# Performance work log

Hardware: AMD Instinct MI355X
Metric: run time of the kernel (lower is better)

Reference implementation:

```python
import jax, jax.numpy as jnp
import numpy as np

VOCAB = 32000
D_MODEL = 512
SEQ_TABLE = 2048
EPS = 1e-5


def layer_norm(x, gamma, beta):
    mu = jnp.mean(x, axis=-1, keepdims=True)
    var = jnp.mean(jnp.square(x - mu), axis=-1, keepdims=True)
    return (x - mu) * jax.lax.rsqrt(var + EPS) * gamma + beta


def setup_inputs() -> dict:
    key = jax.random.key(0)
    ks = jax.random.split(key, 12)
    s = 0.02
    d, h, V = D_MODEL, 4 * D_MODEL, VOCAB
    return {
        "x": jax.random.randint(ks[0], (4, 2048), 0, V, dtype=jnp.int64),
        "word_emb": jax.random.normal(ks[1], (V, d), jnp.float32) * s,
        "pos_emb": jax.random.normal(ks[2], (SEQ_TABLE, d), jnp.float32) * s,
        "Wq": jax.random.normal(ks[3], (d, d), jnp.float32) * s,
        "Wk": jax.random.normal(ks[4], (d, d), jnp.float32) * s,
        "Wv": jax.random.normal(ks[5], (d, d), jnp.float32) * s,
        "g1": jnp.ones((d,), jnp.float32),
        "b1": jnp.zeros((d,), jnp.float32),
        "w_ffn1": jax.random.normal(ks[6], (h, d), jnp.float32) * s,
        "b_ffn1": jnp.zeros((h,), jnp.float32),
        "w_ffn2": jax.random.normal(ks[7], (d, h), jnp.float32) * s,
        "b_ffn2": jnp.zeros((d,), jnp.float32),
        "g2": jnp.ones((d,), jnp.float32),
        "b2": jnp.zeros((d,), jnp.float32),
        "w_vocab": jax.random.normal(ks[8], (V, d), jnp.float32) * s,
        "b_vocab": jnp.zeros((V,), jnp.float32),
    }


def reference(x, word_emb, pos_emb, Wq, Wk, Wv, g1, b1,
              w_ffn1, b_ffn1, w_ffn2, b_ffn2, g2, b2, w_vocab, b_vocab):
    B, S = x.shape
    d_k = Wq.shape[0]
    # embeddings: word + learned positional
    emb = word_emb[x] + pos_emb[jnp.arange(S)][None, :, :]  # [B,S,d]
    # single-head causal attention (torch Linear: y = x @ W.T)
    Q = emb @ Wq.T
    K = emb @ Wk.T
    V = emb @ Wv.T
    scores = jnp.einsum('bqd,bkd->bqk', Q, K) / jnp.sqrt(jnp.float32(d_k))
    causal = jnp.tril(jnp.ones((S, S), bool))
    scores = jnp.where(causal[None], scores, -jnp.inf)
    attn = jax.nn.softmax(scores, axis=-1)
    context = jnp.einsum('bqk,bkd->bqd', attn, V)
    out1 = layer_norm(emb + context, g1, b1)
    ffn = jax.nn.relu(out1 @ w_ffn1.T + b_ffn1) @ w_ffn2.T + b_ffn2
    final = layer_norm(out1 + ffn, g2, b2)
    return final @ w_vocab.T + b_vocab  # [B,S,V]
```

## Files before the change

### kernel.cpp

```cpp
#include <hip/hip_runtime.h>
#include <hip/hip_bf16.h>

typedef __bf16 bf16;
typedef __attribute__((ext_vector_type(4))) __bf16 bf16x4;
typedef __attribute__((ext_vector_type(8))) __bf16 bf16x8;
typedef __attribute__((ext_vector_type(4))) float f32x4;

__device__ inline void gload_lds16(const bf16* g, bf16* l) {
    __builtin_amdgcn_global_load_lds(
        (const __attribute__((address_space(1))) void*)g,
        (__attribute__((address_space(3))) void*)l, 16, 0, 0);
}

struct CvtArgs {
    const float* src[6];
    bf16* dst[6];
    long n4[6];
    float scale[6];
};
__global__ void cvt_all(CvtArgs a) {
    int j = blockIdx.y;
    const float* __restrict__ src = a.src[j];
    bf16* __restrict__ dst = a.dst[j];
    long n4 = a.n4[j];
    float sc = a.scale[j];
    long i = (long)blockIdx.x * blockDim.x + threadIdx.x;
    long stride = (long)gridDim.x * blockDim.x;
    for (; i < n4; i += stride) {
        float4 v = ((const float4*)src)[i];
        bf16x4 o = { (bf16)(v.x * sc), (bf16)(v.y * sc), (bf16)(v.z * sc), (bf16)(v.w * sc) };
        ((bf16x4*)dst)[i] = o;
    }
}

__global__ void embed_kernel(const int* __restrict__ x, const float* __restrict__ we,
                             const float* __restrict__ pe, float* __restrict__ emb_f,
                             bf16* __restrict__ emb_b) {
    int row = blockIdx.x;
    int c   = threadIdx.x;
    int tok = x[row];
    int s   = row & 2047;
    float4 w = ((const float4*)we)[(long)tok * 128 + c];
    float4 p = ((const float4*)pe)[(long)s * 128 + c];
    float4 e = { w.x + p.x, w.y + p.y, w.z + p.z, w.w + p.w };
    ((float4*)emb_f)[(long)row * 128 + c] = e;
    bf16x4 eb = { (bf16)e.x, (bf16)e.y, (bf16)e.z, (bf16)e.w };
    ((bf16x4*)emb_b)[(long)row * 128 + c] = eb;
}

template<bool WF32>
__global__ void ln_kernel(const float* __restrict__ a, const float* __restrict__ bres,
                          const float* __restrict__ g, const float* __restrict__ bb,
                          float* __restrict__ of, bf16* __restrict__ ob) {
    int row = blockIdx.x;
    int t   = threadIdx.x;
    float4 xa = ((const float4*)a)[(long)row * 128 + t];
    float4 xb = ((const float4*)bres)[(long)row * 128 + t];
    float4 xv = { xa.x + xb.x, xa.y + xb.y, xa.z + xb.z, xa.w + xb.w };
    float s  = xv.x + xv.y + xv.z + xv.w;
    float sq = xv.x * xv.x + xv.y * xv.y + xv.z * xv.z + xv.w * xv.w;
    #pragma unroll
    for (int o = 32; o > 0; o >>= 1) {
        s  += __shfl_xor(s, o);
        sq += __shfl_xor(sq, o);
    }
    __shared__ float rs[2], rq[2];
    int wid = t >> 6;
    if ((t & 63) == 0) { rs[wid] = s; rq[wid] = sq; }
    __syncthreads();
    s = rs[0] + rs[1]; sq = rq[0] + rq[1];
    float mu   = s * (1.0f / 512.0f);
    float var  = sq * (1.0f / 512.0f) - mu * mu;
    float rstd = rsqrtf(var + 1e-5f);
    float4 gv = ((const float4*)g)[t];
    float4 bv = ((const float4*)bb)[t];
    float4 y = { (xv.x - mu) * rstd * gv.x + bv.x,
                 (xv.y - mu) * rstd * gv.y + bv.y,
                 (xv.z - mu) * rstd * gv.z + bv.z,
                 (xv.w - mu) * rstd * gv.w + bv.w };
    if (WF32) ((float4*)of)[(long)row * 128 + t] = y;
    bf16x4 yb = { (bf16)y.x, (bf16)y.y, (bf16)y.z, (bf16)y.w };
    ((bf16x4*)ob)[(long)row * 128 + t] = yb;
}

__global__ void softmax_causal(const float* __restrict__ sc, bf16* __restrict__ pr) {
    int row = blockIdx.x;
    int z = row >> 11, q = row & 2047;
    const float* srow = sc + ((long)z * 2048 + q) * 2048;
    bf16*        prow = pr + ((long)z * 2048 + q) * 2048;
    int t = threadIdx.x;
    float v[8];
    int c0 = t * 8;
    if (t <= (q >> 3)) {
        float4 v0 = ((const float4*)srow)[t * 2];
        float4 v1 = ((const float4*)srow)[t * 2 + 1];
        v[0] = v0.x; v[1] = v0.y; v[2] = v0.z; v[3] = v0.w;
        v[4] = v1.x; v[5] = v1.y; v[6] = v1.z; v[7] = v1.w;
    } else {
        #pragma unroll
        for (int j = 0; j < 8; j++) v[j] = -1e30f;
    }
    float mx = -1e30f;
    #pragma unroll
    for (int j = 0; j < 8; j++) {
        if (c0 + j > q) v[j] = -1e30f;
        mx = fmaxf(mx, v[j]);
    }
    int lane = t & 63, wid = t >> 6;
    #pragma unroll
    for (int o = 32; o > 0; o >>= 1) mx = fmaxf(mx, __shfl_xor(mx, o));
    __shared__ float redm[4], reds[4];
    if (lane == 0) redm[wid] = mx;
    __syncthreads();
    mx = fmaxf(fmaxf(redm[0], redm[1]), fmaxf(redm[2], redm[3]));
    float p[8]; float sum = 0.f;
    #pragma unroll
    for (int j = 0; j < 8; j++) {
        p[j] = (c0 + j <= q) ? __expf(v[j] - mx) : 0.f;
        sum += p[j];
    }
    #pragma unroll
    for (int o = 32; o > 0; o >>= 1) sum += __shfl_xor(sum, o);
    if (lane == 0) reds[wid] = sum;
    __syncthreads();
    sum = reds[0] + reds[1] + reds[2] + reds[3];
    float inv = 1.0f / sum;
    int wlim = ((q >> 7) + 1) * 128;
    if (c0 < wlim) {
        bf16x8 o;
        #pragma unroll
        for (int j = 0; j < 8; j++) o[j] = (bf16)(p[j] * inv);
        *(bf16x8*)&prow[c0] = o;
    }
}

enum { EPI_F32 = 0, EPI_BF16 = 1, EPI_VT = 2, EPI_BIAS_RELU_BF16 = 3, EPI_BIAS_F32 = 4,
       EPI_QKV = 5, EPI_BIAS_F32_NT = 6 };
enum { ZB_BATCH = 0 };

template<int EPI, bool CAUSAL_SKIP, bool CAUSAL_K, bool XCD, int ZMODE>
__global__ __launch_bounds__(256)
void gemm_bt(const bf16* __restrict__ A, const bf16* __restrict__ B,
             float* __restrict__ Cf, bf16* __restrict__ Cb,
             const float* __restrict__ bias, float scale,
             int M, int N, int K, int Krow, long sA, long sB, long sC) {
    int br, bc;
    if (XCD) {
        int nwg = gridDim.x * gridDim.y;
        int lin = blockIdx.y * gridDim.x + blockIdx.x;
        lin = (lin & 7) * (nwg >> 3) + (lin >> 3);
        br = lin / gridDim.x; bc = lin - br * gridDim.x;
    } else { br = blockIdx.y; bc = blockIdx.x; }
    int z = blockIdx.z;
    A += (long)z * sA; B += (long)z * sB; Cf += (long)z * sC;
    if (CAUSAL_SKIP && bc > br) return;
    int Kext = CAUSAL_K ? min(K, (br + 1) * 128) : K;
    __shared__ bf16 As[128 * 64];
    __shared__ bf16 Bs[128 * 64];
    int tid = threadIdx.x;
    int lane = tid & 63, wid = tid >> 6;
    int wm = (wid >> 1) * 64, wn = (wid & 1) * 64;
    f32x4 acc[4][4] = {};
    int rowA0 = br * 128, colB0 = bc * 128;
    int rsub = lane >> 3;
    int csub = ((lane & 7) ^ rsub) * 8;
    int rdsw = (lane & 7) * 8;
    for (int kt = 0; kt < Kext; kt += 64) {
        const bf16* Ag = A + (long)rowA0 * Krow + kt;
        const bf16* Bg = B + (long)colB0 * Krow + kt;
        #pragma unroll
        for (int i = 0; i < 4; i++) {
            int seg = wid * 4 + i;
            int r = seg * 8 + rsub;
            gload_lds16(&Ag[(long)r * Krow + csub], &As[seg * 512]);
            gload_lds16(&Bg[(long)r * Krow + csub], &Bs[seg * 512]);
        }
        __syncthreads();
        #pragma unroll
        for (int kk = 0; kk < 2; kk++) {
            bf16x8 af[4], bfr[4];
            int ko = (kk * 32 + (lane >> 4) * 8) ^ rdsw;
            #pragma unroll
            for (int m = 0; m < 4; m++) af[m]  = *(const bf16x8*)&As[(wm + m * 16 + (lane & 15)) * 64 + ko];
            #pragma unroll
            for (int n = 0; n < 4; n++) bfr[n] = *(const bf16x8*)&Bs[(wn + n * 16 + (lane & 15)) * 64 + ko];
            #pragma unroll
            for (int m = 0; m < 4; m++)
                #pragma unroll
                for (int n = 0; n < 4; n++)
                    acc[m][n] = __builtin_amdgcn_mfma_f32_16x16x32_bf16(af[m], bfr[n], acc[m][n], 0, 0, 0);
        }
        __syncthreads();
    }
    #pragma unroll
    for (int m = 0; m < 4; m++) {
        #pragma unroll
        for (int n = 0; n < 4; n++) {
            #pragma unroll
            for (int j = 0; j < 4; j++) {
                int row = rowA0 + wm + m * 16 + (lane >> 4) * 4 + j;
                int col = colB0 + wn + n * 16 + (lane & 15);
                float v = acc[m][n][j];
                if (EPI == EPI_F32) {
                    Cf[(long)row * N + col] = v;
                } else if (EPI == EPI_BF16) {
                    Cb[(long)row * N + col] = (bf16)(v * scale);
                } else if (EPI == EPI_VT) {
                    int b = row >> 11, k = row & 2047;
                    Cb[((long)b * 512 + col) * 2048 + k] = (bf16)v;
                } else if (EPI == EPI_BIAS_RELU_BF16) {
                    float y = fmaxf(v + bias[col], 0.0f);
                    Cb[(long)row * N + col] = (bf16)y;
                } else if (EPI == EPI_BIAS_F32) {
                    Cf[(long)row * N + col] = v + bias[col];
                }
            }
        }
    }
}

template<int EPI, bool XCD, bool CSKIP, int BANDW, int NT>
__global__ __launch_bounds__(512)
void gemm256(const bf16* __restrict__ A, const bf16* __restrict__ B,
             float* __restrict__ Cf, bf16* __restrict__ Cb,
             const float* __restrict__ bias, int N, int K,
             long sA, long sB, long sC) {
    int br, bc;
    if (XCD) {
        int nwg = gridDim.x * gridDim.y;
        int lin = blockIdx.y * gridDim.x + blockIdx.x;
        lin = (lin & 7) * (nwg >> 3) + (lin >> 3);
        if (BANDW > 0) {
            int per = BANDW * gridDim.y;
            int band = lin / per, w2 = lin - band * per;
            br = w2 / BANDW; bc = band * BANDW + (w2 - br * BANDW);
        } else {
            br = lin / gridDim.x; bc = lin - br * gridDim.x;
        }
    } else { br = blockIdx.y; bc = blockIdx.x; }
    if (CSKIP && bc > br) return;
    int z = blockIdx.z;
    A  += (long)z * sA;
    B  += (long)z * sB;
    Cf += (long)z * sC;
    __shared__ bf16 lds[2][2][256 * 64];
    int tid = threadIdx.x;
    int lane = tid & 63, wid = tid >> 6;
    int wm2 = wid >> 2, wn4 = wid & 3;
    long rowA0 = (long)br * 256, colB0 = (long)bc * 256;
    int rsub = lane >> 3;
    int csw  = ((lane & 7) ^ rsub) * 8;
    int l15 = lane & 15;
    int rdxor = (lane & 7) << 3;
    int kbase = (lane >> 4) * 8;
    const bf16* Abase = A + rowA0 * K;
    const bf16* Bbase = B + colB0 * K;
    f32x4 acc[8][4] = {};

    auto stage = [&](int t) {
        int buf = t & 1;
        const bf16* Ag = Abase + t * 64;
        const bf16* Bg = Bbase + t * 64;
        #pragma unroll
        for (int i = 0; i < 4; i++) {
            int seg = wid * 4 + i;
            long r = seg * 8 + rsub;
            gload_lds16(&Ag[r * K + csw], &lds[buf][0][seg * 512]);
        }
        #pragma unroll
        for (int i = 0; i < 4; i++) {
            int seg = wid * 4 + i;
            long r = seg * 8 + rsub;
            gload_lds16(&Bg[r * K + csw], &lds[buf][1][seg * 512]);
        }
    };

    stage(0);
    stage(1);

    for (int t = 0; t < NT; t++) {
        int buf = t & 1;
        if (t == NT - 1) asm volatile("s_waitcnt vmcnt(0)" ::: "memory");
        else             asm volatile("s_waitcnt vmcnt(8)" ::: "memory");
        __builtin_amdgcn_s_barrier();
        const bf16* As = lds[buf][0];
        const bf16* Bs = lds[buf][1];
        bf16x8 bfr[2][4], af[2][4];
        #pragma unroll
        for (int kk = 0; kk < 2; kk++)
            #pragma unroll
            for (int n = 0; n < 4; n++) {
                int r = wn4 * 64 + n * 16 + l15;
                bfr[kk][n] = *(const bf16x8*)&Bs[r * 64 + ((kk * 32 + kbase) ^ rdxor)];
            }
        #pragma unroll
        for (int kk = 0; kk < 2; kk++)
            #pragma unroll
            for (int m = 0; m < 4; m++) {
                int r = wm2 * 128 + m * 16 + l15;
                af[kk][m] = *(const bf16x8*)&As[r * 64 + ((kk * 32 + kbase) ^ rdxor)];
            }
        __builtin_amdgcn_s_setprio(1);
        #pragma unroll
        for (int kk = 0; kk < 2; kk++)
            #pragma unroll
            for (int m = 0; m < 4; m++)
                #pragma unroll
                for (int n = 0; n < 4; n++)
                    acc[m][n] = __builtin_amdgcn_mfma_f32_16x16x32_bf16(af[kk][m], bfr[kk][n], acc[m][n], 0, 0, 0);
        __builtin_amdgcn_s_setprio(0);
        #pragma unroll
        for (int kk = 0; kk < 2; kk++)
            #pragma unroll
            for (int m = 0; m < 4; m++) {
                int r = wm2 * 128 + 64 + m * 16 + l15;
                af[kk][m] = *(const bf16x8*)&As[r * 64 + ((kk * 32 + kbase) ^ rdxor)];
            }
        asm volatile("s_waitcnt lgkmcnt(0)" ::: "memory");
        __builtin_amdgcn_sched_barrier(0);
        __builtin_amdgcn_s_barrier();
        if (t + 2 < NT) stage(t + 2);
        __builtin_amdgcn_s_setprio(1);
        #pragma unroll
        for (int kk = 0; kk < 2; kk++)
            #pragma unroll
            for (int m = 0; m < 4; m++)
                #pragma unroll
                for (int n = 0; n < 4; n++)
                    acc[4 + m][n] = __builtin_amdgcn_mfma_f32_16x16x32_bf16(af[kk][m], bfr[kk][n], acc[4 + m][n], 0, 0, 0);
        __builtin_amdgcn_s_setprio(0);
    }

    if constexpr (EPI == EPI_QKV) {
        int region = (int)(colB0 >> 9);
        if (region < 2) {
            bf16* dst = Cb + (long)region * (8192L * 512);
            int cb = ((int)colB0 & 511) + wn4 * 64;
            #pragma unroll
            for (int m = 0; m < 8; m++)
                #pragma unroll
                for (int n = 0; n < 4; n++)
                    #pragma unroll
                    for (int j = 0; j < 4; j++) {
                        long row = rowA0 + wm2 * 128 + m * 16 + (lane >> 4) * 4 + j;
                        int c = cb + n * 16 + l15;
                        dst[row * 512 + c] = (bf16)acc[m][n][j];
                    }
        } else {
            bf16* vtb = Cb + 2L * 8192 * 512;
            int cb = ((int)colB0 - 1024) + wn4 * 64;
            #pragma unroll
            for (int m = 0; m < 8; m++)
                #pragma unroll
                for (int n = 0; n < 4; n++) {
                    long k0 = rowA0 + wm2 * 128 + m * 16 + (lane >> 4) * 4;
                    long b = k0 >> 11, k = k0 & 2047;
                    int c = cb + n * 16 + l15;
                    bf16x4 pk = { (bf16)acc[m][n][0], (bf16)acc[m][n][1],
                                  (bf16)acc[m][n][2], (bf16)acc[m][n][3] };
                    *(bf16x4*)&vtb[(b * 512 + c) * 2048 + k] = pk;
                }
        }
    } else {
        #pragma unroll
        for (int m = 0; m < 8; m++) {
            #pragma unroll
            for (int n = 0; n < 4; n++) {
                #pragma unroll
                for (int j = 0; j < 4; j++) {
                    long row = rowA0 + wm2 * 128 + m * 16 + (lane >> 4) * 4 + j;
                    long col = colB0 + wn4 * 64 + n * 16 + l15;
                    float v = acc[m][n][j];
                    if (EPI == EPI_BIAS_F32) {
                        Cf[row * N + col] = v + bias[col];
                    } else if (EPI == EPI_BIAS_F32_NT) {
                        __builtin_nontemporal_store(v + bias[col], &Cf[row * N + col]);
                    } else if (EPI == EPI_BIAS_RELU_BF16) {
                        Cb[row * N + col] = (bf16)fmaxf(v + bias[col], 0.0f);
                    } else if (EPI == EPI_F32) {
                        Cf[row * N + col] = v;
                    }
                }
            }
        }
    }
}

extern "C" void kernel_launch(void* const* d_in, const int* in_sizes, int n_in,
                              void* d_out, int out_size, void* d_ws, size_t ws_size,
                              hipStream_t stream) {
    const int*   x       = (const int*)d_in[0];
    const float* word_emb = (const float*)d_in[1];
    const float* pos_emb  = (const float*)d_in[2];
    const float* Wq = (const float*)d_in[3];
    const float* Wk = (const float*)d_in[4];
    const float* Wv = (const float*)d_in[5];
    const float* g1 = (const float*)d_in[6];
    const float* b1 = (const float*)d_in[7];
    const float* w_ffn1 = (const float*)d_in[8];
    const float* b_ffn1 = (const float*)d_in[9];
    const float* w_ffn2 = (const float*)d_in[10];
    const float* b_ffn2 = (const float*)d_in[11];
    const float* g2 = (const float*)d_in[12];
    const float* b2 = (const float*)d_in[13];
    const float* w_vocab = (const float*)d_in[14];
    const float* b_vocab = (const float*)d_in[15];
    float* out = (float*)d_out;

    char* w = (char*)d_ws;
    auto alloc = [&](size_t bytes) { char* p = w; w += (bytes + 255) & ~255ULL; return p; };
    bf16* wqb   = (bf16*)alloc(512 * 512 * 2);
    bf16* wkb   = (bf16*)alloc(512 * 512 * 2);
    bf16* wvb   = (bf16*)alloc(512 * 512 * 2);
    bf16* w1b   = (bf16*)alloc(2048 * 512 * 2);
    bf16* w2b   = (bf16*)alloc(512 * 2048 * 2);
    bf16* wvocb = (bf16*)alloc((size_t)32000 * 512 * 2);
    float* embf = (float*)alloc((size_t)8192 * 512 * 4);
    bf16* embb  = (bf16*)alloc((size_t)8192 * 512 * 2);
    bf16* qb    = (bf16*)alloc((size_t)8192 * 512 * 2);
    bf16* kb    = (bf16*)alloc((size_t)8192 * 512 * 2);
    bf16* vt    = (bf16*)alloc((size_t)8192 * 512 * 2);
    float* scores = (float*)alloc((size_t)4 * 2048 * 2048 * 4);
    bf16* probs = (bf16*)alloc((size_t)4 * 2048 * 2048 * 2);
    float* ctx  = (float*)alloc((size_t)8192 * 512 * 4);
    float* out1f = (float*)alloc((size_t)8192 * 512 * 4);
    float* ffn2f = (float*)alloc((size_t)8192 * 512 * 4);
    bf16* ffn1b = (bf16*)scores;
    bf16* out1b = kb;
    bf16* finalb = embb;

    const float qscale = 0.044194173824159216f;

    CvtArgs ca;
    ca.src[0] = Wq;      ca.dst[0] = wqb;   ca.n4[0] = 512 * 512 / 4;          ca.scale[0] = qscale;
    ca.src[1] = Wk;      ca.dst[1] = wkb;   ca.n4[1] = 512 * 512 / 4;          ca.scale[1] = 1.0f;
    ca.src[2] = Wv;      ca.dst[2] = wvb;   ca.n4[2] = 512 * 512 / 4;          ca.scale[2] = 1.0f;
    ca.src[3] = w_ffn1;  ca.dst[3] = w1b;   ca.n4[3] = 2048 * 512 / 4;         ca.scale[3] = 1.0f;
    ca.src[4] = w_ffn2;  ca.dst[4] = w2b;   ca.n4[4] = 512 * 2048 / 4;         ca.scale[4] = 1.0f;
    ca.src[5] = w_vocab; ca.dst[5] = wvocb; ca.n4[5] = (long)32000 * 512 / 4;  ca.scale[5] = 1.0f;
    cvt_all<<<dim3(256, 6), 256, 0, stream>>>(ca);

    embed_kernel<<<8192, 128, 0, stream>>>(x, word_emb, pos_emb, embf, embb);

    gemm256<EPI_QKV, true, false, 0, 8><<<dim3(6, 32, 1), 512, 0, stream>>>(
        embb, wqb, nullptr, qb, nullptr, 1536, 512, 0, 0, 0);

    gemm256<EPI_F32, true, true, 0, 8><<<dim3(8, 8, 4), 512, 0, stream>>>(
        qb, kb, scores, nullptr, nullptr, 2048, 512,
        (long)2048 * 512, (long)2048 * 512, (long)2048 * 2048);

    softmax_causal<<<8192, 256, 0, stream>>>(scores, probs);

    gemm_bt<EPI_F32, false, true, false, ZB_BATCH><<<dim3(4, 16, 4), 256, 0, stream>>>(
        probs, vt, ctx, nullptr, nullptr, 1.0f, 2048, 512, 2048, 2048,
        (long)2048 * 2048, (long)512 * 2048, (long)2048 * 512);

    ln_kernel<true><<<8192, 128, 0, stream>>>(embf, ctx, g1, b1, out1f, out1b);

    gemm256<EPI_BIAS_RELU_BF16, true, false, 0, 8><<<dim3(8, 32, 1), 512, 0, stream>>>(
        out1b, w1b, nullptr, ffn1b, b_ffn1, 2048, 512, 0, 0, 0);

    gemm_bt<EPI_BIAS_F32, false, false, false, ZB_BATCH><<<dim3(4, 64, 1), 256, 0, stream>>>(
        ffn1b, w2b, ffn2f, nullptr, b_ffn2, 1.0f, 8192, 512, 2048, 2048, 0, 0, 0);

    ln_kernel<false><<<8192, 128, 0, stream>>>(out1f, ffn2f, g2, b2, nullptr, finalb);

    gemm256<EPI_BIAS_F32_NT, true, false, 5, 8><<<dim3(125, 32, 1), 512, 0, stream>>>(
        finalb, wvocb, out, nullptr, b_vocab, 32000, 512, 0, 0, 0);
}
```

Before: 582.0 us.

## Replace vocab projection GEMM with 128x128-tile kernel using banded tile swizzle

Adds a dedicated 128x128-tile bf16 MFMA GEMM for the final vocab projection. It uses double-buffered direct global-to-LDS loads with XOR swizzling and a block remapping that groups tiles into column bands across XCDs. It replaces the 256-wide tile kernel, which launched 4000 workgroups of 512 threads, with 16000 smaller workgroups to improve occupancy, load balance and L2 reuse of the weight matrix. The trade-off is smaller tiles, which means more redundant A/B traffic per output.

Result: faster. 553.8 us (-4.8%).

```diff
diff --git a/kernel.cpp b/kernel.cpp
--- a/kernel.cpp
+++ b/kernel.cpp
@@ -386,6 +386,97 @@
     }
 }
 
+template<int BANDB>
+__global__ __launch_bounds__(256)
+void gemm128v(const bf16* __restrict__ A, const bf16* __restrict__ B,
+              float* __restrict__ C, const float* __restrict__ bias,
+              int N, int K) {
+    const int NBR = 64;
+    const int NT  = 8;
+    int nwg = gridDim.x;
+    int lin = blockIdx.x;
+    lin = (lin & 7) * (nwg >> 3) + (lin >> 3);
+    int per = BANDB * NBR;
+    int band = lin / per, w2 = lin - band * per;
+    int br = w2 / BANDB, bc = band * BANDB + (w2 - br * BANDB);
+
+    __shared__ bf16 lds[2][2][128 * 64];
+    int tid = threadIdx.x;
+    int lane = tid & 63, wid = tid >> 6;
+    int wm = (wid >> 1) * 64, wn = (wid & 1) * 64;
+    int rsub = lane >> 3;
+    int csub = ((lane & 7) ^ rsub) * 8;
+    int rdsw = (lane & 7) * 8;
+    long rowA0 = (long)br * 128, colB0 = (long)bc * 128;
+    const bf16* Abase = A + rowA0 * K;
+    const bf16* Bbase = B + colB0 * K;
+    f32x4 acc[4][4] = {};
+
+    auto stage = [&](int t) {
+        int buf = t & 1;
+        const bf16* Ag = Abase + t * 64;
+        const bf16* Bg = Bbase + t * 64;
+        #pragma unroll
+        for (int i = 0; i < 4; i++) {
+            int seg = wid * 4 + i;
+            long r = seg * 8 + rsub;
+            gload_lds16(&Ag[r * K + csub], &lds[buf][0][seg * 512]);
+        }
+        #pragma unroll
+        for (int i = 0; i < 4; i++) {
+            int seg = wid * 4 + i;
+            long r = seg * 8 + rsub;
+            gload_lds16(&Bg[r * K + csub], &lds[buf][1][seg * 512]);
+        }
+    };
+
+    stage(0);
+    stage(1);
+
+    for (int t = 0; t < NT; t++) {
+        int buf = t & 1;
+        if (t == NT - 1) asm volatile("s_waitcnt vmcnt(0)" ::: "memory");
+        else             asm volatile("s_waitcnt vmcnt(8)" ::: "memory");
+        __builtin_amdgcn_s_barrier();
+        const bf16* As = lds[buf][0];
+        const bf16* Bs = lds[buf][1];
+        __builtin_amdgcn_s_setprio(1);
+        #pragma unroll
+        for (int kk = 0; kk < 2; kk++) {
+            bf16x8 af[4], bfr[4];
+            int ko = (kk * 32 + (lane >> 4) * 8) ^ rdsw;
+            #pragma unroll
+            for (int m = 0; m < 4; m++) af[m]  = *(const bf16x8*)&As[(wm + m * 16 + (lane & 15)) * 64 + ko];
+            #pragma unroll
+            for (int n = 0; n < 4; n++) bfr[n] = *(const bf16x8*)&Bs[(wn + n * 16 + (lane & 15)) * 64 + ko];
+            #pragma unroll
+            for (int m = 0; m < 4; m++)
+                #pragma unroll
+                for (int n = 0; n < 4; n++)
+                    acc[m][n] = __builtin_amdgcn_mfma_f32_16x16x32_bf16(af[m], bfr[n], acc[m][n], 0, 0, 0);
+        }
+        __builtin_amdgcn_s_setprio(0);
+        asm volatile("s_waitcnt lgkmcnt(0)" ::: "memory");
+        __builtin_amdgcn_sched_barrier(0);
+        __builtin_amdgcn_s_barrier();
+        if (t + 2 < NT) stage(t + 2);
+    }
+
+    #pragma unroll
+    for (int m = 0; m < 4; m++) {
+        #pragma unroll
+        for (int n = 0; n < 4; n++) {
+            int col = (int)colB0 + wn + n * 16 + (lane & 15);
+            float bcol = bias[col];
+            #pragma unroll
+            for (int j = 0; j < 4; j++) {
+                long row = rowA0 + wm + m * 16 + (lane >> 4) * 4 + j;
+                __builtin_nontemporal_store(acc[m][n][j] + bcol, &C[row * N + col]);
+            }
+        }
+    }
+}
+
 extern "C" void kernel_launch(void* const* d_in, const int* in_sizes, int n_in,
                               void* d_out, int out_size, void* d_ws, size_t ws_size,
                               hipStream_t stream) {
@@ -465,6 +556,5 @@
 
     ln_kernel<false><<<8192, 128, 0, stream>>>(out1f, ffn2f, g2, b2, nullptr, finalb);
 
-    gemm256<EPI_BIAS_F32_NT, true, false, 5, 8><<<dim3(125, 32, 1), 512, 0, stream>>>(
-        finalb, wvocb, out, nullptr, b_vocab, 32000, 512, 0, 0, 0);
-}
+    gemm128v<10><<<16000, 256, 0, stream>>>(finalb, wvocb, out, b_vocab, 32000, 512);
+}
```

## Replace 256x256 GEMM kernel with 128x128 tiles and banded vocab GEMM

Applied to the files above, without the earlier changes.

Removes the 512-thread 256x256-tile GEMM. The QKV, QK^T and FFN1 GEMMs now run on the existing 128x128 gemm_bt kernel, which gains a QKV epilogue that includes a transposed V write. A new 128x128 gemm128v kernel with XCD remapping and band swizzling handles the vocab projection, hoists the bias load out of the row loop, and writes output with nontemporal stores. Smaller tiles give more workgroups and better occupancy, but each tile reuses less data and issues more global loads.

New measurement: 560.9 us. 3.6% less time.

```diff
diff --git a/kernel.cpp b/kernel.cpp
--- a/kernel.cpp
+++ b/kernel.cpp
@@ -192,70 +192,90 @@
         }
         __syncthreads();
     }
-    #pragma unroll
-    for (int m = 0; m < 4; m++) {
-        #pragma unroll
-        for (int n = 0; n < 4; n++) {
-            #pragma unroll
-            for (int j = 0; j < 4; j++) {
-                int row = rowA0 + wm + m * 16 + (lane >> 4) * 4 + j;
-                int col = colB0 + wn + n * 16 + (lane & 15);
-                float v = acc[m][n][j];
-                if (EPI == EPI_F32) {
-                    Cf[(long)row * N + col] = v;
-                } else if (EPI == EPI_BF16) {
-                    Cb[(long)row * N + col] = (bf16)(v * scale);
-                } else if (EPI == EPI_VT) {
-                    int b = row >> 11, k = row & 2047;
-                    Cb[((long)b * 512 + col) * 2048 + k] = (bf16)v;
-                } else if (EPI == EPI_BIAS_RELU_BF16) {
-                    float y = fmaxf(v + bias[col], 0.0f);
-                    Cb[(long)row * N + col] = (bf16)y;
-                } else if (EPI == EPI_BIAS_F32) {
-                    Cf[(long)row * N + col] = v + bias[col];
+    if constexpr (EPI == EPI_QKV) {
+        int region = colB0 >> 9;
+        if (region < 2) {
+            bf16* dst = Cb + (long)region * (8192L * 512);
+            int cb0 = (colB0 & 511) + wn;
+            #pragma unroll
+            for (int m = 0; m < 4; m++)
+                #pragma unroll
+                for (int n = 0; n < 4; n++)
+                    #pragma unroll
+                    for (int j = 0; j < 4; j++) {
+                        long row = rowA0 + wm + m * 16 + (lane >> 4) * 4 + j;
+                        int c = cb0 + n * 16 + (lane & 15);
+                        dst[row * 512 + c] = (bf16)acc[m][n][j];
+                    }
+        } else {
+            bf16* vtb = Cb + 2L * 8192 * 512;
+            int cb0 = (colB0 - 1024) + wn;
+            #pragma unroll
+            for (int m = 0; m < 4; m++)
+                #pragma unroll
+                for (int n = 0; n < 4; n++) {
+                    long k0 = rowA0 + wm + m * 16 + (lane >> 4) * 4;
+                    long b = k0 >> 11, k = k0 & 2047;
+                    int c = cb0 + n * 16 + (lane & 15);
+                    bf16x4 pk = { (bf16)acc[m][n][0], (bf16)acc[m][n][1],
+                                  (bf16)acc[m][n][2], (bf16)acc[m][n][3] };
+                    *(bf16x4*)&vtb[(b * 512 + c) * 2048 + k] = pk;
+                }
+        }
+    } else {
+        #pragma unroll
+        for (int m = 0; m < 4; m++) {
+            #pragma unroll
+            for (int n = 0; n < 4; n++) {
+                #pragma unroll
+                for (int j = 0; j < 4; j++) {
+                    int row = rowA0 + wm + m * 16 + (lane >> 4) * 4 + j;
+                    int col = colB0 + wn + n * 16 + (lane & 15);
+                    float v = acc[m][n][j];
+                    if (EPI == EPI_F32) {
+                        Cf[(long)row * N + col] = v;
+                    } else if (EPI == EPI_BF16) {
+                        Cb[(long)row * N + col] = (bf16)(v * scale);
+                    } else if (EPI == EPI_VT) {
+                        int b = row >> 11, k = row & 2047;
+                        Cb[((long)b * 512 + col) * 2048 + k] = (bf16)v;
+                    } else if (EPI == EPI_BIAS_RELU_BF16) {
+                        float y = fmaxf(v + bias[col], 0.0f);
+                        Cb[(long)row * N + col] = (bf16)y;
+                    } else if (EPI == EPI_BIAS_F32) {
+                        Cf[(long)row * N + col] = v + bias[col];
+                    }
                 }
             }
         }
     }
 }
 
-template<int EPI, bool XCD, bool CSKIP, int BANDW, int NT>
-__global__ __launch_bounds__(512)
-void gemm256(const bf16* __restrict__ A, const bf16* __restrict__ B,
-             float* __restrict__ Cf, bf16* __restrict__ Cb,
-             const float* __restrict__ bias, int N, int K,
-             long sA, long sB, long sC) {
-    int br, bc;
-    if (XCD) {
-        int nwg = gridDim.x * gridDim.y;
-        int lin = blockIdx.y * gridDim.x + blockIdx.x;
-        lin = (lin & 7) * (nwg >> 3) + (lin >> 3);
-        if (BANDW > 0) {
-            int per = BANDW * gridDim.y;
-            int band = lin / per, w2 = lin - band * per;
-            br = w2 / BANDW; bc = band * BANDW + (w2 - br * BANDW);
-        } else {
-            br = lin / gridDim.x; bc = lin - br * gridDim.x;
-        }
-    } else { br = blockIdx.y; bc = blockIdx.x; }
-    if (CSKIP && bc > br) return;
-    int z = blockIdx.z;
-    A  += (long)z * sA;
-    B  += (long)z * sB;
-    Cf += (long)z * sC;
-    __shared__ bf16 lds[2][2][256 * 64];
+template<int BANDB>
+__global__ __launch_bounds__(256)
+void gemm128v(const bf16* __restrict__ A, const bf16* __restrict__ B,
+              float* __restrict__ C, const float* __restrict__ bias,
+              int N, int K) {
+    const int NBR = 64;
+    const int NT  = 8;
+    int nwg = gridDim.x;
+    int lin = blockIdx.x;
+    lin = (lin & 7) * (nwg >> 3) + (lin >> 3);
+    int per = BANDB * NBR;
+    int band = lin / per, w2 = lin - band * per;
+    int br = w2 / BANDB, bc = band * BANDB + (w2 - br * BANDB);
+
+    __shared__ bf16 lds[2][2][128 * 64];
     int tid = threadIdx.x;
     int lane = tid & 63, wid = tid >> 6;
-    int wm2 = wid >> 2, wn4 = wid & 3;
-    long rowA0 = (long)br * 256, colB0 = (long)bc * 256;
+    int wm = (wid >> 1) * 64, wn = (wid & 1) * 64;
     int rsub = lane >> 3;
-    int csw  = ((lane & 7) ^ rsub) * 8;
-    int l15 = lane & 15;
-    int rdxor = (lane & 7) << 3;
-    int kbase = (lane >> 4) * 8;
+    int csub = ((lane & 7) ^ rsub) * 8;
+    int rdsw = (lane & 7) * 8;
+    long rowA0 = (long)br * 128, colB0 = (long)bc * 128;
     const bf16* Abase = A + rowA0 * K;
     const bf16* Bbase = B + colB0 * K;
-    f32x4 acc[8][4] = {};
+    f32x4 acc[4][4] = {};
 
     auto stage = [&](int t) {
         int buf = t & 1;
@@ -265,13 +285,13 @@
         for (int i = 0; i < 4; i++) {
             int seg = wid * 4 + i;
             long r = seg * 8 + rsub;
-            gload_lds16(&Ag[r * K + csw], &lds[buf][0][seg * 512]);
+            gload_lds16(&Ag[r * K + csub], &lds[buf][0][seg * 512]);
         }
         #pragma unroll
         for (int i = 0; i < 4; i++) {
             int seg = wid * 4 + i;
             long r = seg * 8 + rsub;
-            gload_lds16(&Bg[r * K + csw], &lds[buf][1][seg * 512]);
+            gload_lds16(&Bg[r * K + csub], &lds[buf][1][seg * 512]);
         }
     };
 
@@ -285,102 +305,38 @@
         __builtin_amdgcn_s_barrier();
         const bf16* As = lds[buf][0];
         const bf16* Bs = lds[buf][1];
-        bf16x8 bfr[2][4], af[2][4];
-        #pragma unroll
-        for (int kk = 0; kk < 2; kk++)
-            #pragma unroll
-            for (int n = 0; n < 4; n++) {
-                int r = wn4 * 64 + n * 16 + l15;
-                bfr[kk][n] = *(const bf16x8*)&Bs[r * 64 + ((kk * 32 + kbase) ^ rdxor)];
-            }
-        #pragma unroll
-        for (int kk = 0; kk < 2; kk++)
-            #pragma unroll
-            for (int m = 0; m < 4; m++) {
-                int r = wm2 * 128 + m * 16 + l15;
-                af[kk][m] = *(const bf16x8*)&As[r * 64 + ((kk * 32 + kbase) ^ rdxor)];
-            }
         __builtin_amdgcn_s_setprio(1);
         #pragma unroll
-        for (int kk = 0; kk < 2; kk++)
+        for (int kk = 0; kk < 2; kk++) {
+            bf16x8 af[4], bfr[4];
+            int ko = (kk * 32 + (lane >> 4) * 8) ^ rdsw;
+            #pragma unroll
+            for (int m = 0; m < 4; m++) af[m]  = *(const bf16x8*)&As[(wm + m * 16 + (lane & 15)) * 64 + ko];
+            #pragma unroll
+            for (int n = 0; n < 4; n++) bfr[n] = *(const bf16x8*)&Bs[(wn + n * 16 + (lane & 15)) * 64 + ko];
             #pragma unroll
             for (int m = 0; m < 4; m++)
                 #pragma unroll
                 for (int n = 0; n < 4; n++)
-                    acc[m][n] = __builtin_amdgcn_mfma_f32_16x16x32_bf16(af[kk][m], bfr[kk][n], acc[m][n], 0, 0, 0);
+                    acc[m][n] = __builtin_amdgcn_mfma_f32_16x16x32_bf16(af[m], bfr[n], acc[m][n], 0, 0, 0);
+        }
         __builtin_amdgcn_s_setprio(0);
-        #pragma unroll
-        for (int kk = 0; kk < 2; kk++)
-            #pragma unroll
-            for (int m = 0; m < 4; m++) {
-                int r = wm2 * 128 + 64 + m * 16 + l15;
-                af[kk][m] = *(const bf16x8*)&As[r * 64 + ((kk * 32 + kbase) ^ rdxor)];
-            }
         asm volatile("s_waitcnt lgkmcnt(0)" ::: "memory");
         __builtin_amdgcn_sched_barrier(0);
         __builtin_amdgcn_s_barrier();
         if (t + 2 < NT) stage(t + 2);
-        __builtin_amdgcn_s_setprio(1);
-        #pragma unroll
-        for (int kk = 0; kk < 2; kk++)
-            #pragma unroll
-            for (int m = 0; m < 4; m++)
-                #pragma unroll
-                for (int n = 0; n < 4; n++)
-                    acc[4 + m][n] = __builtin_amdgcn_mfma_f32_16x16x32_bf16(af[kk][m], bfr[kk][n], acc[4 + m][n], 0, 0, 0);
-        __builtin_amdgcn_s_setprio(0);
-    }
-
-    if constexpr (EPI == EPI_QKV) {
-        int region = (int)(colB0 >> 9);
-        if (region < 2) {
-            bf16* dst = Cb + (long)region * (8192L * 512);
-            int cb = ((int)colB0 & 511) + wn4 * 64;
-            #pragma unroll
-            for (int m = 0; m < 8; m++)
-                #pragma unroll
-                for (int n = 0; n < 4; n++)
-                    #pragma unroll
-                    for (int j = 0; j < 4; j++) {
-                        long row = rowA0 + wm2 * 128 + m * 16 + (lane >> 4) * 4 + j;
-                        int c = cb + n * 16 + l15;
-                        dst[row * 512 + c] = (bf16)acc[m][n][j];
-                    }
-        } else {
-            bf16* vtb = Cb + 2L * 8192 * 512;
-            int cb = ((int)colB0 - 1024) + wn4 * 64;
-            #pragma unroll
-            for (int m = 0; m < 8; m++)
-                #pragma unroll
-                for (int n = 0; n < 4; n++) {
-                    long k0 = rowA0 + wm2 * 128 + m * 16 + (lane >> 4) * 4;
-                    long b = k0 >> 11, k = k0 & 2047;
-                    int c = cb + n * 16 + l15;
-                    bf16x4 pk = { (bf16)acc[m][n][0], (bf16)acc[m][n][1],
-                                  (bf16)acc[m][n][2], (bf16)acc[m][n][3] };
-                    *(bf16x4*)&vtb[(b * 512 + c) * 2048 + k] = pk;
-                }
-        }
-    } else {
-        #pragma unroll
-        for (int m = 0; m < 8; m++) {
-            #pragma unroll
-            for (int n = 0; n < 4; n++) {
-                #pragma unroll
-                for (int j = 0; j < 4; j++) {
-                    long row = rowA0 + wm2 * 128 + m * 16 + (lane >> 4) * 4 + j;
-                    long col = colB0 + wn4 * 64 + n * 16 + l15;
-                    float v = acc[m][n][j];
-                    if (EPI == EPI_BIAS_F32) {
-                        Cf[row * N + col] = v + bias[col];
-                    } else if (EPI == EPI_BIAS_F32_NT) {
-                        __builtin_nontemporal_store(v + bias[col], &Cf[row * N + col]);
-                    } else if (EPI == EPI_BIAS_RELU_BF16) {
-                        Cb[row * N + col] = (bf16)fmaxf(v + bias[col], 0.0f);
-                    } else if (EPI == EPI_F32) {
-                        Cf[row * N + col] = v;
-                    }
-                }
+    }
+
+    #pragma unroll
+    for (int m = 0; m < 4; m++) {
+        #pragma unroll
+        for (int n = 0; n < 4; n++) {
+            int col = (int)colB0 + wn + n * 16 + (lane & 15);
+            float bcol = bias[col];
+            #pragma unroll
+            for (int j = 0; j < 4; j++) {
+                long row = rowA0 + wm + m * 16 + (lane >> 4) * 4 + j;
+                __builtin_nontemporal_store(acc[m][n][j] + bcol, &C[row * N + col]);
             }
         }
     }
@@ -442,11 +398,11 @@
 
     embed_kernel<<<8192, 128, 0, stream>>>(x, word_emb, pos_emb, embf, embb);
 
-    gemm256<EPI_QKV, true, false, 0, 8><<<dim3(6, 32, 1), 512, 0, stream>>>(
-        embb, wqb, nullptr, qb, nullptr, 1536, 512, 0, 0, 0);
-
-    gemm256<EPI_F32, true, true, 0, 8><<<dim3(8, 8, 4), 512, 0, stream>>>(
-        qb, kb, scores, nullptr, nullptr, 2048, 512,
+    gemm_bt<EPI_QKV, false, false, true, ZB_BATCH><<<dim3(12, 64, 1), 256, 0, stream>>>(
+        embb, wqb, nullptr, qb, nullptr, 1.0f, 8192, 1536, 512, 512, 0, 0, 0);
+
+    gemm_bt<EPI_F32, true, false, false, ZB_BATCH><<<dim3(16, 16, 4), 256, 0, stream>>>(
+        qb, kb, scores, nullptr, nullptr, 1.0f, 2048, 2048, 512, 512,
         (long)2048 * 512, (long)2048 * 512, (long)2048 * 2048);
 
     softmax_causal<<<8192, 256, 0, stream>>>(scores, probs);
@@ -457,14 +413,13 @@
 
     ln_kernel<true><<<8192, 128, 0, stream>>>(embf, ctx, g1, b1, out1f, out1b);
 
-    gemm256<EPI_BIAS_RELU_BF16, true, false, 0, 8><<<dim3(8, 32, 1), 512, 0, stream>>>(
-        out1b, w1b, nullptr, ffn1b, b_ffn1, 2048, 512, 0, 0, 0);
+    gemm_bt<EPI_BIAS_RELU_BF16, false, false, true, ZB_BATCH><<<dim3(16, 64, 1), 256, 0, stream>>>(
+        out1b, w1b, nullptr, ffn1b, b_ffn1, 1.0f, 8192, 2048, 512, 512, 0, 0, 0);
 
     gemm_bt<EPI_BIAS_F32, false, false, false, ZB_BATCH><<<dim3(4, 64, 1), 256, 0, stream>>>(
         ffn1b, w2b, ffn2f, nullptr, b_ffn2, 1.0f, 8192, 512, 2048, 2048, 0, 0, 0);
 
     ln_kernel<false><<<8192, 128, 0, stream>>>(out1f, ffn2f, g2, b2, nullptr, finalb);
 
-    gemm256<EPI_BIAS_F32_NT, true, false, 5, 8><<<dim3(125, 32, 1), 512, 0, stream>>>(
-        finalb, wvocb, out, nullptr, b_vocab, 32000, 512, 0, 0, 0);
-}
+    gemm128v<10><<<16000, 256, 0, stream>>>(finalb, wvocb, out, b_vocab, 32000, 512);
+}
```
